# Kernel optimization log

Hardware: AMD Instinct MI355X
Metric: run time of the kernel (lower is better)

## Reference

```python
import jax, jax.numpy as jnp
import numpy as np

NUM_CLASSES = 64
EPSILON = 0.05
BETA1 = 1.0
BETA2 = 1.0
WARM_UP_EPOCH = 10


def _loss(x):
    # log_loss: log(1+exp(-(x-eps))) + log(1+exp(x+eps))
    return jax.nn.softplus(-(x - EPSILON)) + jax.nn.softplus(x + EPSILON)


def _per_class_fac(Y):
    # fac_c = 1 / (N_c * (N_total - N_c)); guarded against degenerate classes
    n = Y.sum(0)
    tot = n.sum()
    ok = (n > 0) & (n < tot)
    return jnp.where(ok, 1.0 / jnp.where(ok, n * (tot - n), 1.0), 0.0)


def _masked_pair_sum(x_cij, Y):
    # x_cij: [C,N,N] pairwise arg; Y: [N,C] one-hot. Sum loss over (pos i, neg j)
    pos = Y.T          # [C,N]
    neg = 1.0 - Y.T    # [C,N]
    return jnp.einsum('cij,ci,cj->c', _loss(x_cij), pos, neg)


def _empirical(preds, Y):
    p = preds.T                              # [C,N]
    d = p[:, :, None] - p[:, None, :]        # [C,N,N] delta_f
    per = _masked_pair_sum(4.0 * (1.0 - d), Y)
    return jnp.sum(_per_class_fac(Y) * per)


def _discrepancy(preds, preds_adv, Y):
    p = preds.T
    pa = preds_adv.T
    d = p[:, :, None] - p[:, None, :]        # delta_f
    da = pa[:, :, None] - pa[:, None, :]     # delta_f_hat
    per = _masked_pair_sum(2.0 * (da - d), Y)
    return jnp.sum(_per_class_fac(Y) * per)


def setup_inputs() -> dict:
    key = jax.random.key(0)
    ks = jax.random.split(key, 5)
    N = 1024
    return {
        'y_s': jax.random.normal(ks[0], (N, NUM_CLASSES), jnp.float32),
        'y_s_adv': jax.random.normal(ks[1], (N, NUM_CLASSES), jnp.float32),
        'labels_s': jax.random.randint(ks[2], (N,), 0, NUM_CLASSES),
        'y_t': jax.random.normal(ks[3], (N, NUM_CLASSES), jnp.float32),
        'y_t_adv': jax.random.normal(ks[4], (N, NUM_CLASSES), jnp.float32),
        'epoch': 10,
    }


def reference(y_s, y_s_adv, labels_s, y_t, y_t_adv, epoch):
    ps = jax.nn.softmax(y_s, axis=-1)
    psa = jax.nn.softmax(y_s_adv, axis=-1)
    Ys = jax.nn.one_hot(labels_s, NUM_CLASSES, dtype=ps.dtype)

    empirical = _empirical(ps, Ys)                      # source empirical AUC error
    src_disc = _discrepancy(ps, psa, Ys)
    transfer = -BETA2 * 0.5 * src_disc

    if epoch >= WARM_UP_EPOCH:  # epoch is a static Python int
        pt = jax.nn.softmax(y_t, axis=-1)
        pta = jax.nn.softmax(y_t_adv, axis=-1)
        # pseudo labels: one-hot of argmax of adversarial-head target probs
        Yt = jax.nn.one_hot(jnp.argmax(pta, axis=-1), NUM_CLASSES, dtype=pt.dtype)
        transfer = transfer + BETA1 * 0.25 * _discrepancy(pt, pta, Yt)

    return (0.25 * empirical, transfer)
```

## Files before the change

### kernel.cpp

```cpp
#include <hip/hip_runtime.h>

#define N 1024
#define C 64

__device__ __forceinline__ float loss_f(float x) {
    return __logf((1.0f + __expf(0.05f - x)) * (1.0f + __expf(x + 0.05f)));
}

__global__ __launch_bounds__(1024) void fused_kernel(
    const float* __restrict__ y_s, const float* __restrict__ y_s_adv,
    const int* __restrict__ labels_s,
    const float* __restrict__ y_t, const float* __restrict__ y_t_adv,
    const int* __restrict__ epoch, float* __restrict__ out)
{
    const int c    = blockIdx.x & 63;
    const int term = blockIdx.x >> 6;
    const int tid  = threadIdx.x;
    const int r    = tid;

    __shared__ float sh_col[N];
    __shared__ int   sh_lab[N];
    __shared__ int   sh_pos[N];
    __shared__ int   sh_cnt;
    __shared__ float sh_red[16];
    if (tid == 0) sh_cnt = 0;

    {
        const float* A = (term == 2) ? y_t : y_s;
        const float4* rowA = (const float4*)(A + r * C);
        float sum = 0.0f;
        #pragma unroll
        for (int q = 0; q < 16; ++q) {
            float4 v = rowA[q];
            sum += (__expf(v.x) + __expf(v.y)) + (__expf(v.z) + __expf(v.w));
        }
        float col = __expf(A[r * C + c]) / sum;
        int lab;
        if (term == 0) {
            lab = labels_s[r];
        } else {
            const float* B = (term == 1) ? y_s_adv : y_t_adv;
            const float4* rowB = (const float4*)(B + r * C);
            float sumb = 0.0f;
            float vmax = -1e30f; int imax = 0;
            #pragma unroll
            for (int q = 0; q < 16; ++q) {
                float4 v = rowB[q];
                sumb += (__expf(v.x) + __expf(v.y)) + (__expf(v.z) + __expf(v.w));
                if (term == 2) {
                    if (v.x > vmax) { vmax = v.x; imax = 4 * q + 0; }
                    if (v.y > vmax) { vmax = v.y; imax = 4 * q + 1; }
                    if (v.z > vmax) { vmax = v.z; imax = 4 * q + 2; }
                    if (v.w > vmax) { vmax = v.w; imax = 4 * q + 3; }
                }
            }
            col = __expf(B[r * C + c]) / sumb - col;
            lab = (term == 1) ? labels_s[r] : imax;
        }
        sh_col[r] = col;
        sh_lab[r] = lab;
    }
    __syncthreads();

    if (sh_lab[r] == c) { int k = atomicAdd(&sh_cnt, 1); sh_pos[k] = r; }
    __syncthreads();

    const int n_c = sh_cnt;
    const bool ok = (n_c > 0) && (n_c < N);

    float acc = 0.0f;
    if (ok) {
        const int total = n_c * N;
        for (int p = tid; p < total; p += 1024) {
            const int j = p & (N - 1);
            if (sh_lab[j] == c) continue;
            const float d = sh_col[sh_pos[p >> 10]] - sh_col[j];
            const float arg = (term == 0) ? 4.0f * (1.0f - d) : 2.0f * d;
            acc += loss_f(arg);
        }
    }

    #pragma unroll
    for (int off = 32; off; off >>= 1) acc += __shfl_down(acc, off, 64);
    if ((tid & 63) == 0) sh_red[tid >> 6] = acc;
    __syncthreads();
    if (tid == 0 && ok) {
        float tot = 0.0f;
        #pragma unroll
        for (int w = 0; w < 16; ++w) tot += sh_red[w];
        const float fac = 1.0f / ((float)n_c * (float)(N - n_c));
        float scale;
        int slot;
        if (term == 0)      { scale = 0.25f * fac; slot = 0; }
        else if (term == 1) { scale = -0.5f * fac; slot = 1; }
        else { scale = (epoch[0] >= 10) ? 0.25f * fac : 0.0f; slot = 1; }
        atomicAdd(&out[slot], scale * tot);
    }
}

extern "C" void kernel_launch(void* const* d_in, const int* in_sizes, int n_in,
                              void* d_out, int out_size, void* d_ws, size_t ws_size,
                              hipStream_t stream) {
    const float* y_s     = (const float*)d_in[0];
    const float* y_s_adv = (const float*)d_in[1];
    const int*   labels  = (const int*)d_in[2];
    const float* y_t     = (const float*)d_in[3];
    const float* y_t_adv = (const float*)d_in[4];
    const int*   epoch   = (const int*)d_in[5];

    fused_kernel<<<3 * C, 1024, 0, stream>>>(y_s, y_s_adv, labels,
                                             y_t, y_t_adv, epoch,
                                             (float*)d_out);
}
```

Before: 88.05 us.

## Factor exponentials of pairwise loss into per-sample precomputed terms

Each pairwise loss term is rewritten as log(1 + e^{2eps} + a*e^{m x_i}/e^{m x_j} + b*e^{m x_j}/e^{m x_i}), with the per-sample exponentials and their reciprocals precomputed once into shared memory. The inner loop then needs only a log and two FMAs per pair instead of two exps and a log. The loop is also restructured so each thread owns a fixed negative sample j and iterates over the positives. This drops the per-iteration label check and index math. Precomputing exponentials risks overflow or precision loss for large inputs, though softmax outputs are bounded here.

```diff
diff --git a/kernel.cpp b/kernel.cpp
--- a/kernel.cpp
+++ b/kernel.cpp
@@ -3,9 +3,10 @@
 #define N 1024
 #define C 64
 
-__device__ __forceinline__ float loss_f(float x) {
-    return __logf((1.0f + __expf(0.05f - x)) * (1.0f + __expf(x + 0.05f)));
-}
+#define A2   1.1051709180756477f
+#define AE4  57.397457045447450f
+#define AEM4 0.0192548374188443f
+#define AEPS 1.0512710963760241f
 
 __global__ __launch_bounds__(1024) void fused_kernel(
     const float* __restrict__ y_s, const float* __restrict__ y_s_adv,
@@ -18,7 +19,8 @@
     const int tid  = threadIdx.x;
     const int r    = tid;
 
-    __shared__ float sh_col[N];
+    __shared__ float sh_p[N];
+    __shared__ float sh_q[N];
     __shared__ int   sh_lab[N];
     __shared__ int   sh_pos[N];
     __shared__ int   sh_cnt;
@@ -26,21 +28,21 @@
     if (tid == 0) sh_cnt = 0;
 
     {
-        const float* A = (term == 2) ? y_t : y_s;
-        const float4* rowA = (const float4*)(A + r * C);
+        const float* Am = (term == 2) ? y_t : y_s;
+        const float4* rowA = (const float4*)(Am + r * C);
         float sum = 0.0f;
         #pragma unroll
         for (int q = 0; q < 16; ++q) {
             float4 v = rowA[q];
             sum += (__expf(v.x) + __expf(v.y)) + (__expf(v.z) + __expf(v.w));
         }
-        float col = __expf(A[r * C + c]) / sum;
+        float col = __expf(Am[r * C + c]) / sum;
         int lab;
         if (term == 0) {
             lab = labels_s[r];
         } else {
-            const float* B = (term == 1) ? y_s_adv : y_t_adv;
-            const float4* rowB = (const float4*)(B + r * C);
+            const float* Bm = (term == 1) ? y_s_adv : y_t_adv;
+            const float4* rowB = (const float4*)(Bm + r * C);
             float sumb = 0.0f;
             float vmax = -1e30f; int imax = 0;
             #pragma unroll
@@ -54,10 +56,13 @@
                     if (v.w > vmax) { vmax = v.w; imax = 4 * q + 3; }
                 }
             }
-            col = __expf(B[r * C + c]) / sumb - col;
+            col = __expf(Bm[r * C + c]) / sumb - col;
             lab = (term == 1) ? labels_s[r] : imax;
         }
-        sh_col[r] = col;
+        const float m = (term == 0) ? 4.0f : 2.0f;
+        float e = __expf(m * col);
+        sh_p[r]   = e;
+        sh_q[r]   = 1.0f / e;
         sh_lab[r] = lab;
     }
     __syncthreads();
@@ -69,14 +74,15 @@
     const bool ok = (n_c > 0) && (n_c < N);
 
     float acc = 0.0f;
-    if (ok) {
-        const int total = n_c * N;
-        for (int p = tid; p < total; p += 1024) {
-            const int j = p & (N - 1);
-            if (sh_lab[j] == c) continue;
-            const float d = sh_col[sh_pos[p >> 10]] - sh_col[j];
-            const float arg = (term == 0) ? 4.0f * (1.0f - d) : 2.0f * d;
-            acc += loss_f(arg);
+    if (ok && sh_lab[tid] != c) {
+        const float cA = (term == 0) ? AE4  : AEPS;
+        const float cB = (term == 0) ? AEM4 : AEPS;
+        const float pj = cA * sh_p[tid];
+        const float qj = cB * sh_q[tid];
+        const float base = 1.0f + A2;
+        for (int i = 0; i < n_c; ++i) {
+            const int ip = sh_pos[i];
+            acc += __logf(fmaf(sh_q[ip], pj, fmaf(sh_p[ip], qj, base)));
         }
     }
 
```

Result: faster. 84.14 us (-4.4%).
